# Kernel tuning notes

Measured on AMD Instinct MI355X. Metric: run time of the kernel, lower is better.

The kernel has to match this reference:

```python
import jax, jax.numpy as jnp
import numpy as np

B_SZ, L, H, N, OUT = 16, 4096, 128, 64, 128  # batch, seq, channels(input_dim), state(hidden_dim), output_dim


def _hippo_legs(n):
    # HiPPO-LegS matrix: A[i,k] = -sqrt(2i+1)sqrt(2k+1) for i>k, -(i+1) on diag, 0 above.
    q = np.sqrt(2 * np.arange(n) + 1.0)
    A = -np.tril(np.outer(q, q), -1) - np.diag(np.arange(n) + 1.0)
    return A.astype(np.float32)


def setup_inputs() -> dict:
    key = jax.random.key(0)
    k1, k2, k3, k4, k5, k6, k7 = jax.random.split(key, 7)
    x = jax.random.normal(k1, (B_SZ, L, H), dtype=jnp.float32)
    A = jnp.asarray(_hippo_legs(N))                                   # (N, N) fixed HiPPO
    Bm = jax.random.normal(k2, (H, N), dtype=jnp.float32)             # per-channel input matrix
    Cm = jax.random.normal(k3, (H, N), dtype=jnp.float32)             # per-channel output matrix
    D = jax.random.normal(k4, (H,), dtype=jnp.float32)                # skip/feedthrough
    # log-uniform timescales in [1e-3, 1e-1]
    log_dt = jnp.log(jnp.float32(1e-3)) + jax.random.uniform(k5, (H,), dtype=jnp.float32) * (
        jnp.log(jnp.float32(1e-1)) - jnp.log(jnp.float32(1e-3)))
    W = jax.random.normal(k6, (OUT, H), dtype=jnp.float32) / np.sqrt(H)  # Linear(in=H, out=OUT) weight
    b = jax.random.normal(k7, (OUT,), dtype=jnp.float32) * 0.01
    return {"x": x, "A": A, "Bm": Bm, "Cm": Cm, "D": D, "log_dt": log_dt, "W": W, "b": b}


def reference(x, A, Bm, Cm, D, log_dt, W, b):
    n = A.shape[0]
    seq_len = x.shape[1]
    dt = jnp.exp(log_dt)[:, None, None]            # (H,1,1)
    I = jnp.eye(n, dtype=x.dtype)
    lhs = I[None] - 0.5 * dt * A[None]             # (H,N,N)
    rhs = I[None] + 0.5 * dt * A[None]
    A_bar = jnp.linalg.solve(lhs, rhs)             # bilinear discretization, per channel
    B_bar = jnp.linalg.solve(lhs, (dt[:, :, 0] * Bm)[..., None])[..., 0]  # (H,N)

    # SSM convolution kernel k_l = C A_bar^l B_bar via scan, vectorized over channels.
    def step(V, _):
        k = jnp.einsum('hn,hn->h', Cm, V)
        V = jnp.einsum('hmn,hn->hm', A_bar, V)
        return V, k

    _, ks = jax.lax.scan(step, B_bar, None, length=seq_len)  # (L, H)
    kernel = ks.T                                            # (H, L)

    # Causal convolution via FFT (the 'fourier' method).
    n_fft = 2 * seq_len
    Uf = jnp.fft.rfft(x, n=n_fft, axis=1)                    # (B, F, H)
    Kf = jnp.fft.rfft(kernel, n=n_fft, axis=1)               # (H, F)
    y = jnp.fft.irfft(Uf * Kf.T[None], n=n_fft, axis=1)[:, :seq_len, :]
    y = y + x * D[None, None, :]

    return y @ W.T + b
```

## Files before the change

kernel.cpp:

```cpp
#include <hip/hip_runtime.h>

#define BSZ   16
#define LSEQ  4096
#define HCH   128
#define NST   64
#define NOUTD 128
#define TCH   64
#define NCHK  64

typedef unsigned long long u64;

#define OFF_XT 0ull
#define OFF_U  8388608ull
#define OFF_S  16777216ull
#define OFF_G  25165824ull
#define OFF_M  25690112ull
#define OFF_P  26214400ull
#define OFF_K  26738688ull
#define OFF_WT 26746880ull

__global__ __launch_bounds__(256) void k_tr_x(const float* __restrict__ x, float* __restrict__ xT){
  __shared__ float tile[64][65];
  int l0 = blockIdx.x*64, h0 = blockIdx.y*64, b = blockIdx.z;
  int tid = threadIdx.x;
  int tl = tid>>6, th = tid&63;
  #pragma unroll
  for (int k=0;k<16;k++){
    int l = tl + k*4;
    tile[l][th] = x[((u64)b*LSEQ + l0+l)*HCH + h0+th];
  }
  __syncthreads();
  #pragma unroll
  for (int k=0;k<16;k++){
    int hh = tl + k*4;
    xT[((u64)b*HCH + h0+hh)*LSEQ + l0+th] = tile[th][hh];
  }
}

__global__ __launch_bounds__(256) void k_tr_w(const float* __restrict__ W, float* __restrict__ Wt){
  int idx = blockIdx.x*256 + threadIdx.x;
  int o = idx >> 7, h = idx & 127;
  Wt[h*NOUTD + o] = W[o*HCH + h];
}

__global__ __launch_bounds__(512) void k_pre(const float* __restrict__ A, const float* __restrict__ Bm,
                   const float* __restrict__ Cm, const float* __restrict__ log_dt,
                   float* __restrict__ G, float* __restrict__ Mx,
                   float* __restrict__ P, float* __restrict__ ks){
  __shared__ __align__(16) float Ls [64][68];
  __shared__ __align__(16) float LsT[64][68];
  __shared__ __align__(16) float Bb [64][68];
  __shared__ __align__(16) float BbT[64][68];
  __shared__ __align__(16) float Vt [64][68];
  __shared__ __align__(16) float Wt [64][68];
  __shared__ float vbuf[64];
  __shared__ float cbuf[64];
  const int h = blockIdx.x, tid = threadIdx.x;
  const int lane = tid & 63, wid = tid >> 6;
  const float dt = expf(log_dt[h]);

  for (int i = tid; i < 4096; i += 512){
    int r = i >> 6, c = i & 63;
    Ls[r][c] = ((r==c)?1.f:0.f) - 0.5f*dt*A[i];
  }
  if (tid < 64) vbuf[tid] = Bm[h*NST + tid];
  else if (tid < 128) cbuf[tid-64] = Cm[h*NST + (tid-64)];
  __syncthreads();

  float y[64];
  if (wid == 0){
    const int t = lane;
    #pragma unroll
    for (int j=0;j<64;j++) y[j] = 0.f;
    #pragma unroll
    for (int i=0;i<64;i++){
      float acc = ((i==t)?2.f:0.f) - Ls[i][t];
      #pragma unroll
      for (int j4=0;j4<(i+3)/4;j4++){
        float4 L4 = *(const float4*)&Ls[i][j4*4];
        acc -= L4.x*y[j4*4+0] + L4.y*y[j4*4+1] + L4.z*y[j4*4+2] + L4.w*y[j4*4+3];
      }
      y[i] = acc * (1.0f/Ls[i][i]);
    }
    #pragma unroll
    for (int i=0;i<64;i++){ Ls[i][t] = y[i]; LsT[t][i] = y[i]; }
  }
  __syncthreads();

  if (wid == 0){
    const int t = lane;
    float a0=0.f,a1=0.f,a2=0.f,a3=0.f;
    #pragma unroll
    for (int m4=0;m4<16;m4++){
      float4 r4 = *(const float4*)&Ls[t][m4*4];
      a0 += r4.x*vbuf[m4*4+0]; a1 += r4.y*vbuf[m4*4+1];
      a2 += r4.z*vbuf[m4*4+2]; a3 += r4.w*vbuf[m4*4+3];
    }
    Vt[0][t] = 0.5f*dt*(((a0+a1)+(a2+a3)) + vbuf[t]);
  } else if (wid == 1){
    const int n = lane;
    float a0=0.f,a1=0.f,a2=0.f,a3=0.f;
    #pragma unroll
    for (int m4=0;m4<16;m4++){
      float4 c4 = *(const float4*)&LsT[n][m4*4];
      a0 += c4.x*cbuf[m4*4+0]; a1 += c4.y*cbuf[m4*4+1];
      a2 += c4.z*cbuf[m4*4+2]; a3 += c4.w*cbuf[m4*4+3];
    }
    Wt[0][n] = (a0+a1)+(a2+a3);
  }
  __syncthreads();

  float (*cur)[68]  = Ls,  (*curT)[68] = LsT;
  float (*nxt)[68]  = Bb,  (*nxtT)[68] = BbT;
  for (int k=0;k<6;k++){
    const int nv = 1<<k;
    for (int j = tid; j < 32*nv; j += 512){
      const int isW = (j >= 16*nv);
      const int jj  = isW ? (j - 16*nv) : j;
      const int i   = jj >> 4;
      const int n0  = (jj & 15) << 2;
      float (*Xs)[68] = isW ? Wt  : Vt;
      float (*Ms)[68] = isW ? cur : curT;
      float o0=0.f,o1=0.f,o2=0.f,o3=0.f;
      #pragma unroll
      for (int m4=0;m4<16;m4++){
        const float4 xv = *(const float4*)&Xs[i][m4*4];
        const float4 c0 = *(const float4*)&Ms[m4*4+0][n0];
        const float4 c1 = *(const float4*)&Ms[m4*4+1][n0];
        const float4 c2 = *(const float4*)&Ms[m4*4+2][n0];
        const float4 c3 = *(const float4*)&Ms[m4*4+3][n0];
        o0 += xv.x*c0.x + xv.y*c1.x + xv.z*c2.x + xv.w*c3.x;
        o1 += xv.x*c0.y + xv.y*c1.y + xv.z*c2.y + xv.w*c3.y;
        o2 += xv.x*c0.z + xv.y*c1.z + xv.z*c2.z + xv.w*c3.z;
        o3 += xv.x*c0.w + xv.y*c1.w + xv.z*c2.w + xv.w*c3.w;
      }
      float* dst = isW ? &Wt[nv+i][n0] : &Vt[nv+i][n0];
      *(float4*)dst = make_float4(o0,o1,o2,o3);
    }
    {
      const int ti = (tid >> 4) << 1;
      const int tj = (tid & 15) << 2;
      float acc[2][4] = {};
      #pragma unroll
      for (int m4=0;m4<16;m4++){
        const float4 a0 = *(const float4*)&cur[ti+0][m4*4];
        const float4 a1 = *(const float4*)&cur[ti+1][m4*4];
        const float4 b0 = *(const float4*)&cur[m4*4+0][tj];
        const float4 b1 = *(const float4*)&cur[m4*4+1][tj];
        const float4 b2 = *(const float4*)&cur[m4*4+2][tj];
        const float4 b3 = *(const float4*)&cur[m4*4+3][tj];
        acc[0][0] += a0.x*b0.x + a0.y*b1.x + a0.z*b2.x + a0.w*b3.x;
        acc[0][1] += a0.x*b0.y + a0.y*b1.y + a0.z*b2.y + a0.w*b3.y;
        acc[0][2] += a0.x*b0.z + a0.y*b1.z + a0.z*b2.z + a0.w*b3.z;
        acc[0][3] += a0.x*b0.w + a0.y*b1.w + a0.z*b2.w + a0.w*b3.w;
        acc[1][0] += a1.x*b0.x + a1.y*b1.x + a1.z*b2.x + a1.w*b3.x;
        acc[1][1] += a1.x*b0.y + a1.y*b1.y + a1.z*b2.y + a1.w*b3.y;
        acc[1][2] += a1.x*b0.z + a1.y*b1.z + a1.z*b2.z + a1.w*b3.z;
        acc[1][3] += a1.x*b0.w + a1.y*b1.w + a1.z*b2.w + a1.w*b3.w;
      }
      *(float4*)&nxt[ti+0][tj] = make_float4(acc[0][0],acc[0][1],acc[0][2],acc[0][3]);
      *(float4*)&nxt[ti+1][tj] = make_float4(acc[1][0],acc[1][1],acc[1][2],acc[1][3]);
      #pragma unroll
      for (int e=0;e<4;e++){
        nxtT[tj+e][ti+0] = acc[0][e];
        nxtT[tj+e][ti+1] = acc[1][e];
      }
    }
    __syncthreads();
    { float (*t0)[68]=cur; cur=nxt;  nxt=t0; }
    { float (*t1)[68]=curT; curT=nxtT; nxtT=t1; }
  }

  if (wid == 0){
    const int j = lane;
    float a0=0.f,a1=0.f,a2=0.f,a3=0.f;
    #pragma unroll
    for (int n4=0;n4<16;n4++){
      float4 v4 = *(const float4*)&Vt[j][n4*4];
      a0 += v4.x*cbuf[n4*4+0]; a1 += v4.y*cbuf[n4*4+1];
      a2 += v4.z*cbuf[n4*4+2]; a3 += v4.w*cbuf[n4*4+3];
    }
    ks[h*64 + j] = (a0+a1)+(a2+a3);
  }
  for (int idx = tid; idx < 4096; idx += 512){
    const int t = idx >> 6, n = idx & 63;
    G [(u64)h*4096 + idx] = Vt[63-t][n];
    Mx[(u64)h*4096 + idx] = Wt[t][n];
    P [(u64)h*4096 + idx] = cur[t][n];
  }
}

__global__ __launch_bounds__(256) void k_proj_u(const float* __restrict__ xT, const float* __restrict__ G,
                          float* __restrict__ U){
  int h = blockIdx.x, bc0 = blockIdx.y*64;
  __shared__ __align__(16) float xs[64][65];
  __shared__ __align__(16) float gs[64][68];
  int tid = threadIdx.x;
  for (int i=tid;i<4096;i+=256){
    int t = i>>6, n = i&63;
    gs[t][n] = G[(u64)h*4096 + i];
  }
  for (int i=tid;i<4096;i+=256){
    int r = i>>6, t = i&63;
    int bc = bc0 + r, b = bc>>6, c = bc&63;
    xs[r][t] = xT[((u64)b*HCH + h)*LSEQ + c*64 + t];
  }
  __syncthreads();
  int tb = tid>>4, tn = tid&15;
  float acc[4][4] = {};
  #pragma unroll 8
  for (int t=0;t<64;t++){
    float4 g4 = *(const float4*)&gs[t][tn*4];
    #pragma unroll
    for (int r=0;r<4;r++){
      float xv = xs[tb*4+r][t];
      acc[r][0] += xv*g4.x; acc[r][1] += xv*g4.y; acc[r][2] += xv*g4.z; acc[r][3] += xv*g4.w;
    }
  }
  #pragma unroll
  for (int r=0;r<4;r++){
    int bc = bc0 + tb*4 + r, b = bc>>6, c = bc&63;
    float4 o4 = make_float4(acc[r][0],acc[r][1],acc[r][2],acc[r][3]);
    *(float4*)&U[(((u64)b*HCH + h)*NCHK + c)*NST + tn*4] = o4;
  }
}

__global__ __launch_bounds__(256) void k_scan(const float* __restrict__ U, const float* __restrict__ P,
                        float* __restrict__ S){
  int tid = threadIdx.x, lane = tid&63, wid = tid>>6;
  int bh = blockIdx.x*4 + wid;
  int b = bh>>7, h = bh&127;
  const float* Ph = P + (u64)h*4096;
  float prow[64];
  #pragma unroll
  for (int j4=0;j4<16;j4++){
    float4 p4 = *(const float4*)&Ph[lane*64 + j4*4];
    prow[j4*4+0]=p4.x; prow[j4*4+1]=p4.y; prow[j4*4+2]=p4.z; prow[j4*4+3]=p4.w;
  }
  const float* Ub = U + ((u64)b*HCH + h)*(NCHK*NST);
  float*       Sb = S + ((u64)b*HCH + h)*(NCHK*NST);
  float s = 0.f;
  for (int c=0;c<NCHK;c++){
    Sb[c*64 + lane] = s;
    float acc = Ub[c*64 + lane];
    #pragma unroll
    for (int j=0;j<64;j++){
      float sj = __uint_as_float(__builtin_amdgcn_readlane(__float_as_uint(s), j));
      acc += sj * prow[j];
    }
    s = acc;
  }
}

__global__ __launch_bounds__(256) void k_zmix(const float* __restrict__ xT, const float* __restrict__ S,
                        const float* __restrict__ Mx, const float* __restrict__ ks,
                        const float* __restrict__ D, float* __restrict__ zT){
  int h = blockIdx.x, bc0 = blockIdx.y*64;
  __shared__ __align__(16) float xs[64][65];
  __shared__ __align__(16) float ss[64][65];
  __shared__ __align__(16) float bb[128][68];
  __shared__ __align__(16) float kv[64];
  int tid = threadIdx.x;
  if (tid < 64) kv[tid] = ks[h*64 + tid];
  for (int i=tid;i<4096;i+=256){
    int r=i>>6, t=i&63;
    int bc=bc0+r, b=bc>>6, c=bc&63;
    xs[r][t] = xT[((u64)b*HCH + h)*LSEQ + c*64 + t];
    ss[r][t] = S[(((u64)b*HCH + h)*NCHK + c)*NST + t];
  }
  for (int i=tid;i<4096;i+=256){
    int t=i>>6, n=i&63;
    bb[64+n][t] = Mx[(u64)h*4096 + i];
  }
  __syncthreads();
  for (int i=tid;i<4096;i+=256){
    int j=i>>6, t=i&63;
    bb[j][t] = (t>=j)? kv[t-j] : 0.f;
  }
  __syncthreads();
  int tb=tid>>4, tn=tid&15;
  float acc[4][4]={};
  #pragma unroll 4
  for (int kk=0;kk<64;kk++){
    float4 b4 = *(const float4*)&bb[kk][tn*4];
    #pragma unroll
    for (int r=0;r<4;r++){
      float av = xs[tb*4+r][kk];
      acc[r][0]+=av*b4.x; acc[r][1]+=av*b4.y; acc[r][2]+=av*b4.z; acc[r][3]+=av*b4.w;
    }
  }
  #pragma unroll 4
  for (int kk=0;kk<64;kk++){
    float4 b4 = *(const float4*)&bb[64+kk][tn*4];
    #pragma unroll
    for (int r=0;r<4;r++){
      float av = ss[tb*4+r][kk];
      acc[r][0]+=av*b4.x; acc[r][1]+=av*b4.y; acc[r][2]+=av*b4.z; acc[r][3]+=av*b4.w;
    }
  }
  float dv = D[h];
  #pragma unroll
  for (int r=0;r<4;r++){
    int bc=bc0+tb*4+r, b=bc>>6, c=bc&63;
    float4 o4;
    o4.x = acc[r][0] + dv*xs[tb*4+r][tn*4+0];
    o4.y = acc[r][1] + dv*xs[tb*4+r][tn*4+1];
    o4.z = acc[r][2] + dv*xs[tb*4+r][tn*4+2];
    o4.w = acc[r][3] + dv*xs[tb*4+r][tn*4+3];
    *(float4*)&zT[((u64)b*HCH + h)*LSEQ + c*64 + tn*4] = o4;
  }
}

__global__ __launch_bounds__(256) void k_out(const float* __restrict__ zT, const float* __restrict__ Wt,
                       const float* __restrict__ bias, float* __restrict__ out){
  int l0 = blockIdx.x*64, b = blockIdx.y;
  __shared__ __align__(16) float zl[128][64];
  int tid = threadIdx.x;
  for (int i=tid;i<8192;i+=256){
    int hh=i>>6, ll=i&63;
    zl[hh][ll] = zT[((u64)b*HCH + hh)*LSEQ + l0 + ll];
  }
  __syncthreads();
  int lane = tid&63, wid = tid>>6;
  int o = (wid&1)*64 + lane;
  int lq0 = (wid>>1)*32;
  float bo = bias[o];
  float acc[32];
  #pragma unroll
  for (int q=0;q<32;q++) acc[q] = bo;
  #pragma unroll 2
  for (int hh=0;hh<128;hh++){
    float wv = Wt[hh*NOUTD + o];
    #pragma unroll
    for (int q4=0;q4<8;q4++){
      float4 z4 = *(const float4*)&zl[hh][lq0 + q4*4];
      acc[q4*4+0] += wv*z4.x; acc[q4*4+1] += wv*z4.y; acc[q4*4+2] += wv*z4.z; acc[q4*4+3] += wv*z4.w;
    }
  }
  #pragma unroll
  for (int q=0;q<32;q++){
    out[((u64)b*LSEQ + l0 + lq0 + q)*NOUTD + o] = acc[q];
  }
}

extern "C" void kernel_launch(void* const* d_in, const int* in_sizes, int n_in,
                              void* d_out, int out_size, void* d_ws, size_t ws_size,
                              hipStream_t stream){
  const float* x      = (const float*)d_in[0];
  const float* A      = (const float*)d_in[1];
  const float* Bm     = (const float*)d_in[2];
  const float* Cm     = (const float*)d_in[3];
  const float* D      = (const float*)d_in[4];
  const float* log_dt = (const float*)d_in[5];
  const float* W      = (const float*)d_in[6];
  const float* bias   = (const float*)d_in[7];
  float* out = (float*)d_out;
  float* ws  = (float*)d_ws;

  float* xT = ws + OFF_XT;
  float* U  = ws + OFF_U;
  float* S  = ws + OFF_S;
  float* G  = ws + OFF_G;
  float* Mx = ws + OFF_M;
  float* P  = ws + OFF_P;
  float* ks = ws + OFF_K;
  float* Wt = ws + OFF_WT;
  float* zT = U;

  hipLaunchKernelGGL(k_tr_x,   dim3(64,2,16), dim3(256), 0, stream, x, xT);
  hipLaunchKernelGGL(k_tr_w,   dim3(64),      dim3(256), 0, stream, W, Wt);
  hipLaunchKernelGGL(k_pre,    dim3(128),     dim3(512), 0, stream, A, Bm, Cm, log_dt, G, Mx, P, ks);
  hipLaunchKernelGGL(k_proj_u, dim3(128,16),  dim3(256), 0, stream, xT, G, U);
  hipLaunchKernelGGL(k_scan,   dim3(512),     dim3(256), 0, stream, U, P, S);
  hipLaunchKernelGGL(k_zmix,   dim3(128,16),  dim3(256), 0, stream, xT, S, Mx, ks, D, zT);
  hipLaunchKernelGGL(k_out,    dim3(64,16),   dim3(256), 0, stream, zT, Wt, bias, out);
}
```

Before: 292.3 us.

## Fuse chunk projection, state scan and mixing into one per-(batch,channel) kernel

```diff
diff --git a/kernel.cpp b/kernel.cpp
--- a/kernel.cpp
+++ b/kernel.cpp
@@ -185,129 +185,114 @@
   for (int idx = tid; idx < 4096; idx += 512){
     const int t = idx >> 6, n = idx & 63;
     G [(u64)h*4096 + idx] = Vt[63-t][n];
-    Mx[(u64)h*4096 + idx] = Wt[t][n];
+    Mx[(u64)h*4096 + idx] = Wt[n][t];
     P [(u64)h*4096 + idx] = cur[t][n];
   }
 }
 
-__global__ __launch_bounds__(256) void k_proj_u(const float* __restrict__ xT, const float* __restrict__ G,
-                          float* __restrict__ U){
-  int h = blockIdx.x, bc0 = blockIdx.y*64;
-  __shared__ __align__(16) float xs[64][65];
+__global__ __launch_bounds__(256) void k_ssm(const float* __restrict__ xT, const float* __restrict__ G,
+                       const float* __restrict__ MxT, const float* __restrict__ P,
+                       const float* __restrict__ ks, const float* __restrict__ D,
+                       float* __restrict__ zT){
+  __shared__ __align__(16) float xs[64][68];
   __shared__ __align__(16) float gs[64][68];
-  int tid = threadIdx.x;
-  for (int i=tid;i<4096;i+=256){
-    int t = i>>6, n = i&63;
-    gs[t][n] = G[(u64)h*4096 + i];
-  }
-  for (int i=tid;i<4096;i+=256){
-    int r = i>>6, t = i&63;
-    int bc = bc0 + r, b = bc>>6, c = bc&63;
-    xs[r][t] = xT[((u64)b*HCH + h)*LSEQ + c*64 + t];
-  }
-  __syncthreads();
-  int tb = tid>>4, tn = tid&15;
-  float acc[4][4] = {};
-  #pragma unroll 8
-  for (int t=0;t<64;t++){
-    float4 g4 = *(const float4*)&gs[t][tn*4];
+  __shared__ __align__(16) float ms[64][68];
+  __shared__ __align__(16) float us[64][68];
+  __shared__ float kv[64];
+  const int h = blockIdx.x, b = blockIdx.y;
+  const int tid = threadIdx.x, lane = tid & 63, wid = tid >> 6;
+
+  const float* xb = xT + ((u64)b*HCH + h)*LSEQ;
+  if (tid < 64) kv[tid] = ks[h*64 + tid];
+  for (int i = tid; i < 4096; i += 256){
+    xs[i>>6][i&63] = xb[i];
+    gs[i>>6][i&63] = G  [(u64)h*4096 + i];
+    ms[i>>6][i&63] = MxT[(u64)h*4096 + i];
+  }
+  __syncthreads();
+
+  const int tb = tid>>4, tn = tid&15;
+  {
+    float acc[4][4] = {};
+    #pragma unroll 8
+    for (int t=0;t<64;t++){
+      float4 g4 = *(const float4*)&gs[t][tn*4];
+      #pragma unroll
+      for (int r=0;r<4;r++){
+        float xv = xs[tb*4+r][t];
+        acc[r][0] += xv*g4.x; acc[r][1] += xv*g4.y; acc[r][2] += xv*g4.z; acc[r][3] += xv*g4.w;
+      }
+    }
+    #pragma unroll
+    for (int r=0;r<4;r++)
+      *(float4*)&us[tb*4+r][tn*4] = make_float4(acc[r][0],acc[r][1],acc[r][2],acc[r][3]);
+  }
+  __syncthreads();
+
+  if (wid != 0){
+    for (int i = tid-64; i < 4096; i += 192){
+      int j = i>>6, t = i&63;
+      gs[j][t] = (t>=j)? kv[t-j] : 0.f;
+    }
+  } else {
+    const float* Ph = P + (u64)h*4096;
+    float prow[64];
+    #pragma unroll
+    for (int j4=0;j4<16;j4++){
+      float4 p4 = *(const float4*)&Ph[lane*64 + j4*4];
+      prow[j4*4+0]=p4.x; prow[j4*4+1]=p4.y; prow[j4*4+2]=p4.z; prow[j4*4+3]=p4.w;
+    }
+    float s = 0.f;
+    for (int c=0;c<NCHK;c++){
+      float u = us[c][lane];
+      us[c][lane] = s;
+      float a0=u, a1=0.f, a2=0.f, a3=0.f;
+      #pragma unroll
+      for (int j4=0;j4<16;j4++){
+        float s0 = __uint_as_float(__builtin_amdgcn_readlane(__float_as_uint(s), j4*4+0));
+        float s1 = __uint_as_float(__builtin_amdgcn_readlane(__float_as_uint(s), j4*4+1));
+        float s2 = __uint_as_float(__builtin_amdgcn_readlane(__float_as_uint(s), j4*4+2));
+        float s3 = __uint_as_float(__builtin_amdgcn_readlane(__float_as_uint(s), j4*4+3));
+        a0 += s0*prow[j4*4+0]; a1 += s1*prow[j4*4+1];
+        a2 += s2*prow[j4*4+2]; a3 += s3*prow[j4*4+3];
+      }
+      s = (a0+a1)+(a2+a3);
+    }
+  }
+  __syncthreads();
+
+  {
+    float acc[4][4] = {};
+    #pragma unroll 4
+    for (int kk=0;kk<64;kk++){
+      float4 b4 = *(const float4*)&gs[kk][tn*4];
+      #pragma unroll
+      for (int r=0;r<4;r++){
+        float av = xs[tb*4+r][kk];
+        acc[r][0]+=av*b4.x; acc[r][1]+=av*b4.y; acc[r][2]+=av*b4.z; acc[r][3]+=av*b4.w;
+      }
+    }
+    #pragma unroll 4
+    for (int kk=0;kk<64;kk++){
+      float4 b4 = *(const float4*)&ms[kk][tn*4];
+      #pragma unroll
+      for (int r=0;r<4;r++){
+        float sv = us[tb*4+r][kk];
+        acc[r][0]+=sv*b4.x; acc[r][1]+=sv*b4.y; acc[r][2]+=sv*b4.z; acc[r][3]+=sv*b4.w;
+      }
+    }
+    const float dv = D[h];
+    float* zb = zT + ((u64)b*HCH + h)*LSEQ;
     #pragma unroll
     for (int r=0;r<4;r++){
-      float xv = xs[tb*4+r][t];
-      acc[r][0] += xv*g4.x; acc[r][1] += xv*g4.y; acc[r][2] += xv*g4.z; acc[r][3] += xv*g4.w;
-    }
-  }
-  #pragma unroll
-  for (int r=0;r<4;r++){
-    int bc = bc0 + tb*4 + r, b = bc>>6, c = bc&63;
-    float4 o4 = make_float4(acc[r][0],acc[r][1],acc[r][2],acc[r][3]);
-    *(float4*)&U[(((u64)b*HCH + h)*NCHK + c)*NST + tn*4] = o4;
-  }
-}
-
-__global__ __launch_bounds__(256) void k_scan(const float* __restrict__ U, const float* __restrict__ P,
-                        float* __restrict__ S){
-  int tid = threadIdx.x, lane = tid&63, wid = tid>>6;
-  int bh = blockIdx.x*4 + wid;
-  int b = bh>>7, h = bh&127;
-  const float* Ph = P + (u64)h*4096;
-  float prow[64];
-  #pragma unroll
-  for (int j4=0;j4<16;j4++){
-    float4 p4 = *(const float4*)&Ph[lane*64 + j4*4];
-    prow[j4*4+0]=p4.x; prow[j4*4+1]=p4.y; prow[j4*4+2]=p4.z; prow[j4*4+3]=p4.w;
-  }
-  const float* Ub = U + ((u64)b*HCH + h)*(NCHK*NST);
-  float*       Sb = S + ((u64)b*HCH + h)*(NCHK*NST);
-  float s = 0.f;
-  for (int c=0;c<NCHK;c++){
-    Sb[c*64 + lane] = s;
-    float acc = Ub[c*64 + lane];
-    #pragma unroll
-    for (int j=0;j<64;j++){
-      float sj = __uint_as_float(__builtin_amdgcn_readlane(__float_as_uint(s), j));
-      acc += sj * prow[j];
-    }
-    s = acc;
-  }
-}
-
-__global__ __launch_bounds__(256) void k_zmix(const float* __restrict__ xT, const float* __restrict__ S,
-                        const float* __restrict__ Mx, const float* __restrict__ ks,
-                        const float* __restrict__ D, float* __restrict__ zT){
-  int h = blockIdx.x, bc0 = blockIdx.y*64;
-  __shared__ __align__(16) float xs[64][65];
-  __shared__ __align__(16) float ss[64][65];
-  __shared__ __align__(16) float bb[128][68];
-  __shared__ __align__(16) float kv[64];
-  int tid = threadIdx.x;
-  if (tid < 64) kv[tid] = ks[h*64 + tid];
-  for (int i=tid;i<4096;i+=256){
-    int r=i>>6, t=i&63;
-    int bc=bc0+r, b=bc>>6, c=bc&63;
-    xs[r][t] = xT[((u64)b*HCH + h)*LSEQ + c*64 + t];
-    ss[r][t] = S[(((u64)b*HCH + h)*NCHK + c)*NST + t];
-  }
-  for (int i=tid;i<4096;i+=256){
-    int t=i>>6, n=i&63;
-    bb[64+n][t] = Mx[(u64)h*4096 + i];
-  }
-  __syncthreads();
-  for (int i=tid;i<4096;i+=256){
-    int j=i>>6, t=i&63;
-    bb[j][t] = (t>=j)? kv[t-j] : 0.f;
-  }
-  __syncthreads();
-  int tb=tid>>4, tn=tid&15;
-  float acc[4][4]={};
-  #pragma unroll 4
-  for (int kk=0;kk<64;kk++){
-    float4 b4 = *(const float4*)&bb[kk][tn*4];
-    #pragma unroll
-    for (int r=0;r<4;r++){
-      float av = xs[tb*4+r][kk];
-      acc[r][0]+=av*b4.x; acc[r][1]+=av*b4.y; acc[r][2]+=av*b4.z; acc[r][3]+=av*b4.w;
-    }
-  }
-  #pragma unroll 4
-  for (int kk=0;kk<64;kk++){
-    float4 b4 = *(const float4*)&bb[64+kk][tn*4];
-    #pragma unroll
-    for (int r=0;r<4;r++){
-      float av = ss[tb*4+r][kk];
-      acc[r][0]+=av*b4.x; acc[r][1]+=av*b4.y; acc[r][2]+=av*b4.z; acc[r][3]+=av*b4.w;
-    }
-  }
-  float dv = D[h];
-  #pragma unroll
-  for (int r=0;r<4;r++){
-    int bc=bc0+tb*4+r, b=bc>>6, c=bc&63;
-    float4 o4;
-    o4.x = acc[r][0] + dv*xs[tb*4+r][tn*4+0];
-    o4.y = acc[r][1] + dv*xs[tb*4+r][tn*4+1];
-    o4.z = acc[r][2] + dv*xs[tb*4+r][tn*4+2];
-    o4.w = acc[r][3] + dv*xs[tb*4+r][tn*4+3];
-    *(float4*)&zT[((u64)b*HCH + h)*LSEQ + c*64 + tn*4] = o4;
+      int c = tb*4+r;
+      float4 o4;
+      o4.x = acc[r][0] + dv*xs[c][tn*4+0];
+      o4.y = acc[r][1] + dv*xs[c][tn*4+1];
+      o4.z = acc[r][2] + dv*xs[c][tn*4+2];
+      o4.w = acc[r][3] + dv*xs[c][tn*4+3];
+      *(float4*)&zb[c*64 + tn*4] = o4;
+    }
   }
 }
 
@@ -357,21 +342,17 @@
   float* out = (float*)d_out;
   float* ws  = (float*)d_ws;
 
-  float* xT = ws + OFF_XT;
-  float* U  = ws + OFF_U;
-  float* S  = ws + OFF_S;
-  float* G  = ws + OFF_G;
-  float* Mx = ws + OFF_M;
-  float* P  = ws + OFF_P;
-  float* ks = ws + OFF_K;
-  float* Wt = ws + OFF_WT;
-  float* zT = U;
-
-  hipLaunchKernelGGL(k_tr_x,   dim3(64,2,16), dim3(256), 0, stream, x, xT);
-  hipLaunchKernelGGL(k_tr_w,   dim3(64),      dim3(256), 0, stream, W, Wt);
-  hipLaunchKernelGGL(k_pre,    dim3(128),     dim3(512), 0, stream, A, Bm, Cm, log_dt, G, Mx, P, ks);
-  hipLaunchKernelGGL(k_proj_u, dim3(128,16),  dim3(256), 0, stream, xT, G, U);
-  hipLaunchKernelGGL(k_scan,   dim3(512),     dim3(256), 0, stream, U, P, S);
-  hipLaunchKernelGGL(k_zmix,   dim3(128,16),  dim3(256), 0, stream, xT, S, Mx, ks, D, zT);
-  hipLaunchKernelGGL(k_out,    dim3(64,16),   dim3(256), 0, stream, zT, Wt, bias, out);
-}
+  float* xT  = ws + OFF_XT;
+  float* zT  = ws + OFF_U;
+  float* G   = ws + OFF_G;
+  float* MxT = ws + OFF_M;
+  float* P   = ws + OFF_P;
+  float* ks  = ws + OFF_K;
+  float* Wt  = ws + OFF_WT;
+
+  hipLaunchKernelGGL(k_tr_x, dim3(64,2,16), dim3(256), 0, stream, x, xT);
+  hipLaunchKernelGGL(k_tr_w, dim3(64),      dim3(256), 0, stream, W, Wt);
+  hipLaunchKernelGGL(k_pre,  dim3(128),     dim3(512), 0, stream, A, Bm, Cm, log_dt, G, MxT, P, ks);
+  hipLaunchKernelGGL(k_ssm,  dim3(128,16),  dim3(256), 0, stream, xT, G, MxT, P, ks, D, zT);
+  hipLaunchKernelGGL(k_out,  dim3(64,16),   dim3(256), 0, stream, zT, Wt, bias, out);
+}
```

Measured after the change: 295.4 us. About the same (+1.1%).
